# Optimization experiments

Measured on AMD Instinct MI355X. Metric: run time of the kernel, lower is better.

The kernel has to match this reference:

```python
import jax, jax.numpy as jnp
import numpy as np
from jax import lax

RADIUS = 8
EPS = 0.01


def box_filter(x, r):
    # Sum over a (2r+1)x(2r+1) window with zero ('same') padding — identical math
    # to depthwise conv2d with a ones kernel and padding=r.
    k = 2 * r + 1
    return lax.reduce_window(
        x, jnp.array(0, x.dtype), lax.add,
        window_dimensions=(1, 1, k, k),
        window_strides=(1, 1, 1, 1),
        padding=((0, 0), (0, 0), (r, r), (r, r)),
    )


def setup_inputs() -> dict:
    key = jax.random.key(0)
    k1, k2 = jax.random.split(key)
    shape = (16, 3, 512, 512)
    I = jax.random.uniform(k1, shape, dtype=jnp.float32)
    p = jax.random.uniform(k2, shape, dtype=jnp.float32)
    return {"I": I, "p": p}


def reference(I, p):
    r = RADIUS
    eps = EPS
    N = box_filter(jnp.ones_like(I), r)          # window pixel counts (handles borders)
    mean_I = box_filter(I, r) / N
    mean_p = box_filter(p, r) / N
    mean_Ip = box_filter(I * p, r) / N
    cov_Ip = mean_Ip - mean_I * mean_p
    mean_II = box_filter(I * I, r) / N
    var_I = mean_II - mean_I * mean_I
    a = cov_Ip / (var_I + eps)
    b = mean_p - a * mean_I
    mean_a = box_filter(a, r) / N
    mean_b = box_filter(b, r) / N
    q = mean_a * I + mean_b
    return q
```

## Files before the change

kernel.cpp:

```cpp
#include <hip/hip_runtime.h>


#define RAD  8
#define H    512
#define W    512
#define TILE 32
#define EPS  0.01f

__global__ __launch_bounds__(512, 4)
void guided_filter_kernel(const float* __restrict__ Ig,
                          const float* __restrict__ Pg,
                          float* __restrict__ out)
{
    __shared__ __align__(16) float4 F4[64 * 32];
    __shared__ __align__(16) float4 H4[64 * 48];

    float2* F2p = (float2*)F4;
    float2* AB  = (float2*)F4;
    float2* HAB = (float2*)F4 + 48 * 50;

    const int tid   = threadIdx.x;
    const int plane = blockIdx.z;
    const int x0 = blockIdx.x * TILE - 2 * RAD;
    const int y0 = blockIdx.y * TILE - 2 * RAD;
    const float* Ib = Ig + (size_t)plane * (H * W);
    const float* Pb = Pg + (size_t)plane * (H * W);
    float* Ob = out + (size_t)plane * (H * W);

    const bool interior = (x0 >= 0) && (y0 >= 0) && (x0 + 64 <= W) && (y0 + 64 <= H);
    if (interior) {
        #pragma unroll
        for (int it = 0; it < 2; ++it) {
            int idx = it * 512 + tid;
            int ry = idx >> 4, f4 = idx & 15;
            int rl = ry & 7, pf = ry & 1;
            const float* ip = Ib + (y0 + ry) * W + x0 + 4 * f4;
            const float* pp = Pb + (y0 + ry) * W + x0 + 4 * f4;
            float4 iv = *(const float4*)ip;
            float4 pv = *(const float4*)pp;
            float2 e0 = make_float2(iv.x, pv.x), e1 = make_float2(iv.y, pv.y);
            float2 e2 = make_float2(iv.z, pv.z), e3 = make_float2(iv.w, pv.w);
            float2 a0 = pf ? e1 : e0, a1 = pf ? e0 : e1;
            float2 b0 = pf ? e3 : e2, b1 = pf ? e2 : e3;
            float4* Fr = &F4[ry * 32];
            Fr[(2 * f4) ^ rl]     = make_float4(a0.x, a0.y, a1.x, a1.y);
            Fr[(2 * f4 + 1) ^ rl] = make_float4(b0.x, b0.y, b1.x, b1.y);
        }
    } else {
        #pragma unroll
        for (int it = 0; it < 2; ++it) {
            int idx = it * 512 + tid;
            int ry = idx >> 4, f4 = idx & 15;
            int rl = ry & 7, pf = ry & 1;
            int gy = y0 + ry;
            float2 el[4];
            #pragma unroll
            for (int k = 0; k < 4; ++k) {
                int gx = x0 + 4 * f4 + k;
                bool v = ((unsigned)gy < (unsigned)H) && ((unsigned)gx < (unsigned)W);
                el[k].x = v ? Ib[gy * W + gx] : 0.f;
                el[k].y = v ? Pb[gy * W + gx] : 0.f;
            }
            float2 a0 = pf ? el[1] : el[0], a1 = pf ? el[0] : el[1];
            float2 b0 = pf ? el[3] : el[2], b1 = pf ? el[2] : el[3];
            float4* Fr = &F4[ry * 32];
            Fr[(2 * f4) ^ rl]     = make_float4(a0.x, a0.y, a1.x, a1.y);
            Fr[(2 * f4 + 1) ^ rl] = make_float4(b0.x, b0.y, b1.x, b1.y);
        }
    }
    __syncthreads();

    {
        const int r  = tid >> 3, e = tid & 7;
        const int rl = r & 7, pf = r & 1;
        const int c0 = 6 * e;
        const float4* Fr = &F4[r * 32];
        const float2* Er = &F2p[r * 64];
        float4 S = make_float4(0.f, 0.f, 0.f, 0.f);
        const int g0 = 3 * e;
        #pragma unroll
        for (int m = 0; m < 8; ++m) {
            float4 g = Fr[(g0 + m) ^ rl];
            S.x += g.x + g.z;
            S.y += g.y + g.w;
            S.z += g.x * g.y + g.z * g.w;
            S.w += g.x * g.x + g.z * g.z;
        }
        {
            int c = c0 + 16;
            float2 v = Er[(((c >> 1) ^ rl) << 1) | pf];
            S.x += v.x; S.y += v.y; S.z += v.x * v.y; S.w += v.x * v.x;
        }
        #pragma unroll
        for (int k = 0; k < 6; ++k) {
            H4[r * 48 + ((c0 + k) ^ rl)] = S;
            if (k < 5) {
                int ca = c0 + k + 17, cs = c0 + k;
                float2 va = Er[(((ca >> 1) ^ rl) << 1) | ((ca & 1) ^ pf)];
                float2 vs = Er[(((cs >> 1) ^ rl) << 1) | ((cs & 1) ^ pf)];
                S.x += va.x - vs.x;
                S.y += va.y - vs.y;
                S.z += va.x * va.y - vs.x * vs.y;
                S.w += va.x * va.x - vs.x * vs.x;
            }
        }
    }
    __syncthreads();

    if (tid < 384) {
        const int col = tid % 48, chunk = tid / 48;
        const int cy0 = chunk * 6;
        float4 S = make_float4(0.f, 0.f, 0.f, 0.f);
        #pragma unroll
        for (int j = 0; j < 17; ++j) {
            int row = cy0 + j;
            float4 v = H4[row * 48 + (col ^ (row & 7))];
            S.x += v.x; S.y += v.y; S.z += v.z; S.w += v.w;
        }
        int gx = x0 + RAD + col;
        int nx = min(gx + RAD, W - 1) - max(gx - RAD, 0) + 1;
        #pragma unroll
        for (int k = 0; k < 6; ++k) {
            int cy = cy0 + k;
            int gy = y0 + RAD + cy;
            float a = 0.f, b = 0.f;
            if (((unsigned)gy < (unsigned)H) && ((unsigned)gx < (unsigned)W)) {
                int ny = min(gy + RAD, H - 1) - max(gy - RAD, 0) + 1;
                float invN = __builtin_amdgcn_rcpf((float)(nx * ny));
                float mI = S.x * invN, mp = S.y * invN;
                float cov = S.z * invN - mI * mp;
                float var = S.w * invN - mI * mI;
                a = cov * __builtin_amdgcn_rcpf(var + EPS);
                b = mp - a * mI;
            }
            AB[cy * 50 + col] = make_float2(a, b);
            if (k < 5) {
                int ra = cy + 17, rs = cy;
                float4 va = H4[ra * 48 + (col ^ (ra & 7))];
                float4 vs = H4[rs * 48 + (col ^ (rs & 7))];
                S.x += va.x - vs.x; S.y += va.y - vs.y;
                S.z += va.z - vs.z; S.w += va.w - vs.w;
            }
        }
    }
    __syncthreads();

    if (tid < 384) {
        const int r = tid % 48, e = tid / 48;
        const int c0 = 4 * e;
        const float2* row  = &AB[r * 50];
        const float4* rowg = (const float4*)row;
        float2 S = make_float2(0.f, 0.f);
        #pragma unroll
        for (int m = 0; m < 8; ++m) {
            float4 g = rowg[2 * e + m];
            S.x += g.x + g.z;
            S.y += g.y + g.w;
        }
        {
            float2 v = row[c0 + 16];
            S.x += v.x; S.y += v.y;
        }
        #pragma unroll
        for (int k = 0; k < 4; ++k) {
            HAB[r * 33 + c0 + k] = S;
            if (k < 3) {
                float2 va = row[c0 + k + 17];
                float2 vs = row[c0 + k];
                S.x += va.x - vs.x; S.y += va.y - vs.y;
            }
        }
    }
    __syncthreads();

    {
        const int col = tid & 31, chunk = tid >> 5;
        const int oy0 = chunk * 2;
        float2 S = make_float2(0.f, 0.f);
        #pragma unroll
        for (int j = 0; j < 17; ++j) {
            float2 v = HAB[(oy0 + j) * 33 + col];
            S.x += v.x; S.y += v.y;
        }
        int gx = x0 + 2 * RAD + col;
        int nx = min(gx + RAD, W - 1) - max(gx - RAD, 0) + 1;
        #pragma unroll
        for (int k = 0; k < 2; ++k) {
            int oy = oy0 + k;
            int gy = y0 + 2 * RAD + oy;
            int ny = min(gy + RAD, H - 1) - max(gy - RAD, 0) + 1;
            float invN = __builtin_amdgcn_rcpf((float)(nx * ny));
            float iv = Ib[gy * W + gx];
            Ob[gy * W + gx] = S.x * invN * iv + S.y * invN;
            if (k < 1) {
                float2 va = HAB[(oy + 17) * 33 + col];
                float2 vs = HAB[oy * 33 + col];
                S.x += va.x - vs.x; S.y += va.y - vs.y;
            }
        }
    }
}

extern "C" void kernel_launch(void* const* d_in, const int* in_sizes, int n_in,
                              void* d_out, int out_size, void* d_ws, size_t ws_size,
                              hipStream_t stream) {
    const float* I = (const float*)d_in[0];
    const float* P = (const float*)d_in[1];
    float* out = (float*)d_out;
    int planes = in_sizes[0] / (H * W);
    dim3 grid(W / TILE, H / TILE, planes);
    guided_filter_kernel<<<grid, dim3(512), 0, stream>>>(I, P, out);
}
```

Before: 247.8 us.

## Stream four vertical tiles per block with a rolling row-sum ring buffer

Each block now processes a column strip of four 32-row tiles. The horizontal row sums are kept in a 64-row ring buffer, so only 32 new raw rows are staged and row-summed per tile instead of recomputing the full 64-row halo. This cuts redundant vertical-halo loads and first-pass box-filter work. The cost is fewer blocks in the grid, which lowers parallelism, plus a serial chain of syncs inside each block.

```diff
diff --git a/kernel.cpp b/kernel.cpp
--- a/kernel.cpp
+++ b/kernel.cpp
@@ -5,6 +5,7 @@
 #define H    512
 #define W    512
 #define TILE 32
+#define KCH  4
 #define EPS  0.01f
 
 __global__ __launch_bounds__(512, 4)
@@ -22,158 +23,165 @@
     const int tid   = threadIdx.x;
     const int plane = blockIdx.z;
     const int x0 = blockIdx.x * TILE - 2 * RAD;
-    const int y0 = blockIdx.y * TILE - 2 * RAD;
+    const int Y0 = blockIdx.y * (TILE * KCH);
     const float* Ib = Ig + (size_t)plane * (H * W);
     const float* Pb = Pg + (size_t)plane * (H * W);
     float* Ob = out + (size_t)plane * (H * W);
 
-    const bool interior = (x0 >= 0) && (y0 >= 0) && (x0 + 64 <= W) && (y0 + 64 <= H);
-    if (interior) {
-        #pragma unroll
-        for (int it = 0; it < 2; ++it) {
-            int idx = it * 512 + tid;
-            int ry = idx >> 4, f4 = idx & 15;
-            int rl = ry & 7, pf = ry & 1;
-            const float* ip = Ib + (y0 + ry) * W + x0 + 4 * f4;
-            const float* pp = Pb + (y0 + ry) * W + x0 + 4 * f4;
-            float4 iv = *(const float4*)ip;
-            float4 pv = *(const float4*)pp;
-            float2 e0 = make_float2(iv.x, pv.x), e1 = make_float2(iv.y, pv.y);
-            float2 e2 = make_float2(iv.z, pv.z), e3 = make_float2(iv.w, pv.w);
-            float2 a0 = pf ? e1 : e0, a1 = pf ? e0 : e1;
-            float2 b0 = pf ? e3 : e2, b1 = pf ? e2 : e3;
-            float4* Fr = &F4[ry * 32];
-            Fr[(2 * f4) ^ rl]     = make_float4(a0.x, a0.y, a1.x, a1.y);
-            Fr[(2 * f4 + 1) ^ rl] = make_float4(b0.x, b0.y, b1.x, b1.y);
-        }
-    } else {
-        #pragma unroll
-        for (int it = 0; it < 2; ++it) {
-            int idx = it * 512 + tid;
-            int ry = idx >> 4, f4 = idx & 15;
-            int rl = ry & 7, pf = ry & 1;
-            int gy = y0 + ry;
-            float2 el[4];
+    auto stage_raw = [&](int ybase, int nrows) {
+        const int iters = (nrows * 16) >> 9;
+        const bool interior = (x0 >= 0) && (x0 + 64 <= W) &&
+                              (ybase >= 0) && (ybase + nrows <= H);
+        if (interior) {
+            for (int it = 0; it < iters; ++it) {
+                int idx = it * 512 + tid;
+                int ry = idx >> 4, f4 = idx & 15;
+                int rl = ry & 7, pf = ry & 1;
+                const float* ip = Ib + (ybase + ry) * W + x0 + 4 * f4;
+                const float* pp = Pb + (ybase + ry) * W + x0 + 4 * f4;
+                float4 iv = *(const float4*)ip;
+                float4 pv = *(const float4*)pp;
+                float2 e0 = make_float2(iv.x, pv.x), e1 = make_float2(iv.y, pv.y);
+                float2 e2 = make_float2(iv.z, pv.z), e3 = make_float2(iv.w, pv.w);
+                float2 a0 = pf ? e1 : e0, a1 = pf ? e0 : e1;
+                float2 b0 = pf ? e3 : e2, b1 = pf ? e2 : e3;
+                float4* Fr = &F4[ry * 32];
+                Fr[(2 * f4) ^ rl]     = make_float4(a0.x, a0.y, a1.x, a1.y);
+                Fr[(2 * f4 + 1) ^ rl] = make_float4(b0.x, b0.y, b1.x, b1.y);
+            }
+        } else {
+            for (int it = 0; it < iters; ++it) {
+                int idx = it * 512 + tid;
+                int ry = idx >> 4, f4 = idx & 15;
+                int rl = ry & 7, pf = ry & 1;
+                int gy = ybase + ry;
+                float2 el[4];
+                #pragma unroll
+                for (int k = 0; k < 4; ++k) {
+                    int gx = x0 + 4 * f4 + k;
+                    bool v = ((unsigned)gy < (unsigned)H) && ((unsigned)gx < (unsigned)W);
+                    el[k].x = v ? Ib[gy * W + gx] : 0.f;
+                    el[k].y = v ? Pb[gy * W + gx] : 0.f;
+                }
+                float2 a0 = pf ? el[1] : el[0], a1 = pf ? el[0] : el[1];
+                float2 b0 = pf ? el[3] : el[2], b1 = pf ? el[2] : el[3];
+                float4* Fr = &F4[ry * 32];
+                Fr[(2 * f4) ^ rl]     = make_float4(a0.x, a0.y, a1.x, a1.y);
+                Fr[(2 * f4 + 1) ^ rl] = make_float4(b0.x, b0.y, b1.x, b1.y);
+            }
+        }
+    };
+
+    auto s2_rows = [&](int tbase, bool full) {
+        if (full || tid < 256) {
+            const int r  = tid >> 3, e = tid & 7;
+            const int rl = r & 7, pf = r & 1;
+            const int c0 = 6 * e;
+            const float4* Fr = &F4[r * 32];
+            const float2* Er = (const float2*)Fr;
+            float4 S = make_float4(0.f, 0.f, 0.f, 0.f);
+            const int gb = 3 * e;
+            #pragma unroll
+            for (int m = 0; m < 8; ++m) {
+                float4 fr = Fr[(gb + m) ^ rl];
+                S.x += fr.x + fr.z;
+                S.y += fr.y + fr.w;
+                S.z += fr.x * fr.y + fr.z * fr.w;
+                S.w += fr.x * fr.x + fr.z * fr.z;
+            }
+            {
+                int c = c0 + 16;
+                float2 v = Er[(((c >> 1) ^ rl) << 1) | pf];
+                S.x += v.x; S.y += v.y; S.z += v.x * v.y; S.w += v.x * v.x;
+            }
+            const int slot = (tbase + r) & 63;
+            float4* Hrow = &H4[slot * 48];
+            #pragma unroll
+            for (int k = 0; k < 6; ++k) {
+                Hrow[(c0 + k) ^ rl] = S;
+                if (k < 5) {
+                    int ca = c0 + k + 17, cs = c0 + k;
+                    float2 va = Er[(((ca >> 1) ^ rl) << 1) | ((ca & 1) ^ pf)];
+                    float2 vs = Er[(((cs >> 1) ^ rl) << 1) | ((cs & 1) ^ pf)];
+                    S.x += va.x - vs.x;
+                    S.y += va.y - vs.y;
+                    S.z += va.x * va.y - vs.x * vs.y;
+                    S.w += va.x * va.x - vs.x * vs.x;
+                }
+            }
+        }
+    };
+
+    auto s3g = [&](int g) {
+        if (tid < 384) {
+            const int col = tid % 48, chunk = tid / 48;
+            const int cy0 = chunk * 6;
+            const int tb = 32 * g;
+            float4 S = make_float4(0.f, 0.f, 0.f, 0.f);
+            #pragma unroll
+            for (int j = 0; j < 17; ++j) {
+                int row = tb + cy0 + j;
+                float4 v = H4[(row & 63) * 48 + (col ^ (row & 7))];
+                S.x += v.x; S.y += v.y; S.z += v.z; S.w += v.w;
+            }
+            int gx = x0 + RAD + col;
+            int nx = min(gx + RAD, W - 1) - max(gx - RAD, 0) + 1;
+            #pragma unroll
+            for (int k = 0; k < 6; ++k) {
+                int cy = cy0 + k;
+                int gy = Y0 + 32 * g - RAD + cy;
+                float a = 0.f, b = 0.f;
+                if (((unsigned)gy < (unsigned)H) && ((unsigned)gx < (unsigned)W)) {
+                    int ny = min(gy + RAD, H - 1) - max(gy - RAD, 0) + 1;
+                    float invN = __builtin_amdgcn_rcpf((float)(nx * ny));
+                    float mI = S.x * invN, mp = S.y * invN;
+                    float cov = S.z * invN - mI * mp;
+                    float var = S.w * invN - mI * mI;
+                    a = cov * __builtin_amdgcn_rcpf(var + EPS);
+                    b = mp - a * mI;
+                }
+                AB[cy * 50 + col] = make_float2(a, b);
+                if (k < 5) {
+                    int ra = tb + cy + 17, rs = tb + cy;
+                    float4 va = H4[(ra & 63) * 48 + (col ^ (ra & 7))];
+                    float4 vs = H4[(rs & 63) * 48 + (col ^ (rs & 7))];
+                    S.x += va.x - vs.x; S.y += va.y - vs.y;
+                    S.z += va.z - vs.z; S.w += va.w - vs.w;
+                }
+            }
+        }
+    };
+
+    auto s4 = [&]() {
+        if (tid < 384) {
+            const int r = tid % 48, e = tid / 48;
+            const int c0 = 4 * e;
+            const float2* row  = &AB[r * 50];
+            const float4* rowg = (const float4*)row;
+            float2 S = make_float2(0.f, 0.f);
+            #pragma unroll
+            for (int m = 0; m < 8; ++m) {
+                float4 gq = rowg[2 * e + m];
+                S.x += gq.x + gq.z;
+                S.y += gq.y + gq.w;
+            }
+            {
+                float2 v = row[c0 + 16];
+                S.x += v.x; S.y += v.y;
+            }
             #pragma unroll
             for (int k = 0; k < 4; ++k) {
-                int gx = x0 + 4 * f4 + k;
-                bool v = ((unsigned)gy < (unsigned)H) && ((unsigned)gx < (unsigned)W);
-                el[k].x = v ? Ib[gy * W + gx] : 0.f;
-                el[k].y = v ? Pb[gy * W + gx] : 0.f;
-            }
-            float2 a0 = pf ? el[1] : el[0], a1 = pf ? el[0] : el[1];
-            float2 b0 = pf ? el[3] : el[2], b1 = pf ? el[2] : el[3];
-            float4* Fr = &F4[ry * 32];
-            Fr[(2 * f4) ^ rl]     = make_float4(a0.x, a0.y, a1.x, a1.y);
-            Fr[(2 * f4 + 1) ^ rl] = make_float4(b0.x, b0.y, b1.x, b1.y);
-        }
-    }
-    __syncthreads();
-
-    {
-        const int r  = tid >> 3, e = tid & 7;
-        const int rl = r & 7, pf = r & 1;
-        const int c0 = 6 * e;
-        const float4* Fr = &F4[r * 32];
-        const float2* Er = &F2p[r * 64];
-        float4 S = make_float4(0.f, 0.f, 0.f, 0.f);
-        const int g0 = 3 * e;
-        #pragma unroll
-        for (int m = 0; m < 8; ++m) {
-            float4 g = Fr[(g0 + m) ^ rl];
-            S.x += g.x + g.z;
-            S.y += g.y + g.w;
-            S.z += g.x * g.y + g.z * g.w;
-            S.w += g.x * g.x + g.z * g.z;
-        }
-        {
-            int c = c0 + 16;
-            float2 v = Er[(((c >> 1) ^ rl) << 1) | pf];
-            S.x += v.x; S.y += v.y; S.z += v.x * v.y; S.w += v.x * v.x;
-        }
-        #pragma unroll
-        for (int k = 0; k < 6; ++k) {
-            H4[r * 48 + ((c0 + k) ^ rl)] = S;
-            if (k < 5) {
-                int ca = c0 + k + 17, cs = c0 + k;
-                float2 va = Er[(((ca >> 1) ^ rl) << 1) | ((ca & 1) ^ pf)];
-                float2 vs = Er[(((cs >> 1) ^ rl) << 1) | ((cs & 1) ^ pf)];
-                S.x += va.x - vs.x;
-                S.y += va.y - vs.y;
-                S.z += va.x * va.y - vs.x * vs.y;
-                S.w += va.x * va.x - vs.x * vs.x;
-            }
-        }
-    }
-    __syncthreads();
-
-    if (tid < 384) {
-        const int col = tid % 48, chunk = tid / 48;
-        const int cy0 = chunk * 6;
-        float4 S = make_float4(0.f, 0.f, 0.f, 0.f);
-        #pragma unroll
-        for (int j = 0; j < 17; ++j) {
-            int row = cy0 + j;
-            float4 v = H4[row * 48 + (col ^ (row & 7))];
-            S.x += v.x; S.y += v.y; S.z += v.z; S.w += v.w;
-        }
-        int gx = x0 + RAD + col;
-        int nx = min(gx + RAD, W - 1) - max(gx - RAD, 0) + 1;
-        #pragma unroll
-        for (int k = 0; k < 6; ++k) {
-            int cy = cy0 + k;
-            int gy = y0 + RAD + cy;
-            float a = 0.f, b = 0.f;
-            if (((unsigned)gy < (unsigned)H) && ((unsigned)gx < (unsigned)W)) {
-                int ny = min(gy + RAD, H - 1) - max(gy - RAD, 0) + 1;
-                float invN = __builtin_amdgcn_rcpf((float)(nx * ny));
-                float mI = S.x * invN, mp = S.y * invN;
-                float cov = S.z * invN - mI * mp;
-                float var = S.w * invN - mI * mI;
-                a = cov * __builtin_amdgcn_rcpf(var + EPS);
-                b = mp - a * mI;
-            }
-            AB[cy * 50 + col] = make_float2(a, b);
-            if (k < 5) {
-                int ra = cy + 17, rs = cy;
-                float4 va = H4[ra * 48 + (col ^ (ra & 7))];
-                float4 vs = H4[rs * 48 + (col ^ (rs & 7))];
-                S.x += va.x - vs.x; S.y += va.y - vs.y;
-                S.z += va.z - vs.z; S.w += va.w - vs.w;
-            }
-        }
-    }
-    __syncthreads();
-
-    if (tid < 384) {
-        const int r = tid % 48, e = tid / 48;
-        const int c0 = 4 * e;
-        const float2* row  = &AB[r * 50];
-        const float4* rowg = (const float4*)row;
-        float2 S = make_float2(0.f, 0.f);
-        #pragma unroll
-        for (int m = 0; m < 8; ++m) {
-            float4 g = rowg[2 * e + m];
-            S.x += g.x + g.z;
-            S.y += g.y + g.w;
-        }
-        {
-            float2 v = row[c0 + 16];
-            S.x += v.x; S.y += v.y;
-        }
-        #pragma unroll
-        for (int k = 0; k < 4; ++k) {
-            HAB[r * 33 + c0 + k] = S;
-            if (k < 3) {
-                float2 va = row[c0 + k + 17];
-                float2 vs = row[c0 + k];
-                S.x += va.x - vs.x; S.y += va.y - vs.y;
-            }
-        }
-    }
-    __syncthreads();
-
-    {
+                HAB[r * 33 + c0 + k] = S;
+                if (k < 3) {
+                    float2 va = row[c0 + k + 17];
+                    float2 vs = row[c0 + k];
+                    S.x += va.x - vs.x; S.y += va.y - vs.y;
+                }
+            }
+        }
+    };
+
+    auto s5g = [&](int g) {
         const int col = tid & 31, chunk = tid >> 5;
         const int oy0 = chunk * 2;
         float2 S = make_float2(0.f, 0.f);
@@ -187,7 +195,7 @@
         #pragma unroll
         for (int k = 0; k < 2; ++k) {
             int oy = oy0 + k;
-            int gy = y0 + 2 * RAD + oy;
+            int gy = Y0 + 32 * g + oy;
             int ny = min(gy + RAD, H - 1) - max(gy - RAD, 0) + 1;
             float invN = __builtin_amdgcn_rcpf((float)(nx * ny));
             float iv = Ib[gy * W + gx];
@@ -198,6 +206,25 @@
                 S.x += va.x - vs.x; S.y += va.y - vs.y;
             }
         }
+    };
+
+    stage_raw(Y0 - 2 * RAD, 64);
+    __syncthreads();
+    s2_rows(0, true);
+    #pragma unroll 1
+    for (int g = 0; g < KCH; ++g) {
+        __syncthreads();
+        s3g(g);
+        __syncthreads();
+        s4();
+        __syncthreads();
+        if (g < KCH - 1)
+            stage_raw(Y0 + 32 * g + 48, 32);
+        s5g(g);
+        if (g < KCH - 1) {
+            __syncthreads();
+            s2_rows(32 * g + 64, false);
+        }
     }
 }
 
@@ -208,6 +235,6 @@
     const float* P = (const float*)d_in[1];
     float* out = (float*)d_out;
     int planes = in_sizes[0] / (H * W);
-    dim3 grid(W / TILE, H / TILE, planes);
+    dim3 grid(W / TILE, H / (TILE * KCH), planes);
     guided_filter_kernel<<<grid, dim3(512), 0, stream>>>(I, P, out);
 }
```

After: 242.4 us. 2.2% less time.

## Stream vertical tile chunks through a ring buffer with warp-specialized pipelined stages

Applied to the files above, without the earlier changes.

Each block now processes four vertically stacked 32-row tiles using a 48-row ring buffer of horizontal sums, so the vertical halo rows are shared instead of recomputed per tile. Thread groups are specialized so that the second box-filter stages of one chunk overlap with loading and first-stage sums of the next. The a/b intermediates are stored as half2 in shared memory to cut LDS footprint, which reduces the precision of the second filter pass. Block size and launch bounds change to 448 threads and 6 waves per EU, and the grid shrinks by the chunk factor.

```diff
diff --git a/kernel.cpp b/kernel.cpp
--- a/kernel.cpp
+++ b/kernel.cpp
@@ -1,203 +1,205 @@
 #include <hip/hip_runtime.h>
+#include <hip/hip_fp16.h>
 
 
 #define RAD  8
 #define H    512
 #define W    512
 #define TILE 32
+#define KCH  4
 #define EPS  0.01f
 
-__global__ __launch_bounds__(512, 4)
+__global__ __launch_bounds__(448, 6)
 void guided_filter_kernel(const float* __restrict__ Ig,
                           const float* __restrict__ Pg,
                           float* __restrict__ out)
 {
-    __shared__ __align__(16) float4 F4[64 * 32];
-    __shared__ __align__(16) float4 H4[64 * 48];
-
-    float2* F2p = (float2*)F4;
-    float2* AB  = (float2*)F4;
-    float2* HAB = (float2*)F4 + 48 * 50;
+    __shared__ __align__(16) float4  RING[48 * 48];
+    __shared__ __align__(8)  __half2 ABR[48 * 51];
+    __shared__ __align__(8)  __half2 HABR[48 * 33];
 
     const int tid   = threadIdx.x;
     const int plane = blockIdx.z;
     const int x0 = blockIdx.x * TILE - 2 * RAD;
-    const int y0 = blockIdx.y * TILE - 2 * RAD;
+    const int Y0 = blockIdx.y * (TILE * KCH);
     const float* Ib = Ig + (size_t)plane * (H * W);
     const float* Pb = Pg + (size_t)plane * (H * W);
     float* Ob = out + (size_t)plane * (H * W);
 
-    const bool interior = (x0 >= 0) && (y0 >= 0) && (x0 + 64 <= W) && (y0 + 64 <= H);
-    if (interior) {
-        #pragma unroll
-        for (int it = 0; it < 2; ++it) {
-            int idx = it * 512 + tid;
-            int ry = idx >> 4, f4 = idx & 15;
-            int rl = ry & 7, pf = ry & 1;
-            const float* ip = Ib + (y0 + ry) * W + x0 + 4 * f4;
-            const float* pp = Pb + (y0 + ry) * W + x0 + 4 * f4;
-            float4 iv = *(const float4*)ip;
-            float4 pv = *(const float4*)pp;
-            float2 e0 = make_float2(iv.x, pv.x), e1 = make_float2(iv.y, pv.y);
-            float2 e2 = make_float2(iv.z, pv.z), e3 = make_float2(iv.w, pv.w);
-            float2 a0 = pf ? e1 : e0, a1 = pf ? e0 : e1;
-            float2 b0 = pf ? e3 : e2, b1 = pf ? e2 : e3;
-            float4* Fr = &F4[ry * 32];
-            Fr[(2 * f4) ^ rl]     = make_float4(a0.x, a0.y, a1.x, a1.y);
-            Fr[(2 * f4 + 1) ^ rl] = make_float4(b0.x, b0.y, b1.x, b1.y);
-        }
-    } else {
-        #pragma unroll
-        for (int it = 0; it < 2; ++it) {
-            int idx = it * 512 + tid;
-            int ry = idx >> 4, f4 = idx & 15;
-            int rl = ry & 7, pf = ry & 1;
-            int gy = y0 + ry;
-            float2 el[4];
+    auto s2f = [&](int T0, int nrows, int tid2) {
+        if (tid2 < nrows * 8) {
+            const int r = tid2 >> 3, e = tid2 & 7;
+            int slot = (T0 % 48) + r; if (slot >= 48) slot -= 48;
+            const int rl = r & 7;
+            const int ty = Y0 + T0 - 16 + r;
+            const int cb = 6 * e;
+            float4 bI[6], bP[6];
+            const bool xint = (x0 >= 0) && (x0 + 64 <= W);
+            if (xint && ((unsigned)ty < (unsigned)H)) {
+                const float* pi = Ib + ty * W + x0 + cb;
+                const float* pp = Pb + ty * W + x0 + cb;
+                #pragma unroll
+                for (int k = 0; k < 6; ++k) {
+                    __builtin_memcpy(&bI[k], pi + 4 * k, 16);
+                    __builtin_memcpy(&bP[k], pp + 4 * k, 16);
+                }
+            } else {
+                const bool vy = (unsigned)ty < (unsigned)H;
+                float* fI = (float*)bI;
+                float* fP = (float*)bP;
+                #pragma unroll
+                for (int c = 0; c < 24; ++c) {
+                    int gx = x0 + cb + c;
+                    bool v = vy && ((unsigned)gx < (unsigned)W);
+                    fI[c] = v ? Ib[ty * W + gx] : 0.f;
+                    fP[c] = v ? Pb[ty * W + gx] : 0.f;
+                }
+            }
+            const float* fI = (const float*)bI;
+            const float* fP = (const float*)bP;
+            float4 S = make_float4(0.f, 0.f, 0.f, 0.f);
+            #pragma unroll
+            for (int c = 0; c <= 16; ++c) {
+                float iv = fI[c], pv = fP[c];
+                S.x += iv; S.y += pv; S.z += iv * pv; S.w += iv * iv;
+            }
+            float4* Hrow = &RING[slot * 48];
+            #pragma unroll
+            for (int k = 0; k < 6; ++k) {
+                Hrow[(cb + k) ^ rl] = S;
+                if (k < 5) {
+                    float ia = fI[17 + k], pa = fP[17 + k];
+                    float is = fI[k],      ps = fP[k];
+                    S.x += ia - is;
+                    S.y += pa - ps;
+                    S.z += ia * pa - is * ps;
+                    S.w += ia * ia - is * is;
+                }
+            }
+        }
+    };
+
+    auto s3 = [&](int AY, int nch) {
+        if (tid < 48 * nch) {
+            const int col = tid % 48;
+            const int ay0 = AY + 8 * (tid / 48);
+            const int base = ay0 % 48;
+            const int tW = 48 - base;
+            const char* Rb = (const char*)RING;
+            unsigned alo[8], ahi[8];
+            #pragma unroll
+            for (int k = 0; k < 8; ++k) {
+                alo[k] = (unsigned)(base * 768 + ((col ^ k) << 4));
+                ahi[k] = alo[k] - 36864u;
+            }
+            float4 S = make_float4(0.f, 0.f, 0.f, 0.f);
+            #pragma unroll
+            for (int j = 0; j < 17; ++j) {
+                unsigned off = (j >= tW ? ahi[j & 7] : alo[j & 7])
+                               + (unsigned)(j * 768);
+                float4 v = *(const float4*)(Rb + off);
+                S.x += v.x; S.y += v.y; S.z += v.z; S.w += v.w;
+            }
+            const int gx = x0 + RAD + col;
+            const int nx = min(gx + RAD, W - 1) - max(gx - RAD, 0) + 1;
+            #pragma unroll
+            for (int kk = 0; kk < 8; ++kk) {
+                int ya = Y0 + ay0 + kk - 8;
+                float a = 0.f, b = 0.f;
+                if (((unsigned)ya < (unsigned)H) && ((unsigned)gx < (unsigned)W)) {
+                    int ny = min(ya + RAD, H - 1) - max(ya - RAD, 0) + 1;
+                    float invN = __builtin_amdgcn_rcpf((float)(nx * ny));
+                    float mI = S.x * invN, mp = S.y * invN;
+                    float cov = S.z * invN - mI * mp;
+                    float var = S.w * invN - mI * mI;
+                    a = cov * __builtin_amdgcn_rcpf(var + EPS);
+                    b = mp - a * mI;
+                }
+                ABR[(base + kk) * 51 + col] = __floats2half2_rn(a, b);
+                if (kk < 7) {
+                    unsigned offs = (kk >= tW ? ahi[kk & 7] : alo[kk & 7])
+                                    + (unsigned)(kk * 768);
+                    int ja = kk + 17;
+                    unsigned offa = (ja >= tW ? ahi[ja & 7] : alo[ja & 7])
+                                    + (unsigned)(ja * 768);
+                    float4 va = *(const float4*)(Rb + offa);
+                    float4 vs = *(const float4*)(Rb + offs);
+                    S.x += va.x - vs.x; S.y += va.y - vs.y;
+                    S.z += va.z - vs.z; S.w += va.w - vs.w;
+                }
+            }
+        }
+    };
+
+    auto s4 = [&](int i) {
+        if (tid < 192) {
+            const int r = tid % 48, e = tid / 48;
+            const int c0 = 8 * e;
+            int slot = (32 * i) % 48 + r; if (slot >= 48) slot -= 48;
+            const __half2* Arow = &ABR[slot * 51];
+            float2 S = make_float2(0.f, 0.f);
+            #pragma unroll
+            for (int d = 0; d <= 16; ++d) {
+                float2 v = __half22float2(Arow[c0 + d]);
+                S.x += v.x; S.y += v.y;
+            }
+            #pragma unroll
+            for (int k = 0; k < 8; ++k) {
+                HABR[r * 33 + c0 + k] = __floats2half2_rn(S.x, S.y);
+                if (k < 7) {
+                    float2 va = __half22float2(Arow[c0 + k + 17]);
+                    float2 vs = __half22float2(Arow[c0 + k]);
+                    S.x += va.x - vs.x; S.y += va.y - vs.y;
+                }
+            }
+        }
+    };
+
+    auto s5 = [&](int i) {
+        if (tid >= 192) {
+            const int t2 = tid - 192;
+            const int qc = t2 & 31, oy0 = (t2 >> 5) * 4;
+            float2 S = make_float2(0.f, 0.f);
+            #pragma unroll
+            for (int j = 0; j < 17; ++j) {
+                float2 v = __half22float2(HABR[(oy0 + j) * 33 + qc]);
+                S.x += v.x; S.y += v.y;
+            }
+            const int gx = x0 + 2 * RAD + qc;
+            const int nx = min(gx + RAD, W - 1) - max(gx - RAD, 0) + 1;
             #pragma unroll
             for (int k = 0; k < 4; ++k) {
-                int gx = x0 + 4 * f4 + k;
-                bool v = ((unsigned)gy < (unsigned)H) && ((unsigned)gx < (unsigned)W);
-                el[k].x = v ? Ib[gy * W + gx] : 0.f;
-                el[k].y = v ? Pb[gy * W + gx] : 0.f;
-            }
-            float2 a0 = pf ? el[1] : el[0], a1 = pf ? el[0] : el[1];
-            float2 b0 = pf ? el[3] : el[2], b1 = pf ? el[2] : el[3];
-            float4* Fr = &F4[ry * 32];
-            Fr[(2 * f4) ^ rl]     = make_float4(a0.x, a0.y, a1.x, a1.y);
-            Fr[(2 * f4 + 1) ^ rl] = make_float4(b0.x, b0.y, b1.x, b1.y);
-        }
-    }
-    __syncthreads();
-
-    {
-        const int r  = tid >> 3, e = tid & 7;
-        const int rl = r & 7, pf = r & 1;
-        const int c0 = 6 * e;
-        const float4* Fr = &F4[r * 32];
-        const float2* Er = &F2p[r * 64];
-        float4 S = make_float4(0.f, 0.f, 0.f, 0.f);
-        const int g0 = 3 * e;
-        #pragma unroll
-        for (int m = 0; m < 8; ++m) {
-            float4 g = Fr[(g0 + m) ^ rl];
-            S.x += g.x + g.z;
-            S.y += g.y + g.w;
-            S.z += g.x * g.y + g.z * g.w;
-            S.w += g.x * g.x + g.z * g.z;
-        }
-        {
-            int c = c0 + 16;
-            float2 v = Er[(((c >> 1) ^ rl) << 1) | pf];
-            S.x += v.x; S.y += v.y; S.z += v.x * v.y; S.w += v.x * v.x;
-        }
-        #pragma unroll
-        for (int k = 0; k < 6; ++k) {
-            H4[r * 48 + ((c0 + k) ^ rl)] = S;
-            if (k < 5) {
-                int ca = c0 + k + 17, cs = c0 + k;
-                float2 va = Er[(((ca >> 1) ^ rl) << 1) | ((ca & 1) ^ pf)];
-                float2 vs = Er[(((cs >> 1) ^ rl) << 1) | ((cs & 1) ^ pf)];
-                S.x += va.x - vs.x;
-                S.y += va.y - vs.y;
-                S.z += va.x * va.y - vs.x * vs.y;
-                S.w += va.x * va.x - vs.x * vs.x;
-            }
-        }
-    }
-    __syncthreads();
-
-    if (tid < 384) {
-        const int col = tid % 48, chunk = tid / 48;
-        const int cy0 = chunk * 6;
-        float4 S = make_float4(0.f, 0.f, 0.f, 0.f);
-        #pragma unroll
-        for (int j = 0; j < 17; ++j) {
-            int row = cy0 + j;
-            float4 v = H4[row * 48 + (col ^ (row & 7))];
-            S.x += v.x; S.y += v.y; S.z += v.z; S.w += v.w;
-        }
-        int gx = x0 + RAD + col;
-        int nx = min(gx + RAD, W - 1) - max(gx - RAD, 0) + 1;
-        #pragma unroll
-        for (int k = 0; k < 6; ++k) {
-            int cy = cy0 + k;
-            int gy = y0 + RAD + cy;
-            float a = 0.f, b = 0.f;
-            if (((unsigned)gy < (unsigned)H) && ((unsigned)gx < (unsigned)W)) {
+                int gy = Y0 + 32 * i + oy0 + k;
                 int ny = min(gy + RAD, H - 1) - max(gy - RAD, 0) + 1;
                 float invN = __builtin_amdgcn_rcpf((float)(nx * ny));
-                float mI = S.x * invN, mp = S.y * invN;
-                float cov = S.z * invN - mI * mp;
-                float var = S.w * invN - mI * mI;
-                a = cov * __builtin_amdgcn_rcpf(var + EPS);
-                b = mp - a * mI;
-            }
-            AB[cy * 50 + col] = make_float2(a, b);
-            if (k < 5) {
-                int ra = cy + 17, rs = cy;
-                float4 va = H4[ra * 48 + (col ^ (ra & 7))];
-                float4 vs = H4[rs * 48 + (col ^ (rs & 7))];
-                S.x += va.x - vs.x; S.y += va.y - vs.y;
-                S.z += va.z - vs.z; S.w += va.w - vs.w;
-            }
-        }
-    }
-    __syncthreads();
-
-    if (tid < 384) {
-        const int r = tid % 48, e = tid / 48;
-        const int c0 = 4 * e;
-        const float2* row  = &AB[r * 50];
-        const float4* rowg = (const float4*)row;
-        float2 S = make_float2(0.f, 0.f);
-        #pragma unroll
-        for (int m = 0; m < 8; ++m) {
-            float4 g = rowg[2 * e + m];
-            S.x += g.x + g.z;
-            S.y += g.y + g.w;
-        }
-        {
-            float2 v = row[c0 + 16];
-            S.x += v.x; S.y += v.y;
-        }
-        #pragma unroll
-        for (int k = 0; k < 4; ++k) {
-            HAB[r * 33 + c0 + k] = S;
-            if (k < 3) {
-                float2 va = row[c0 + k + 17];
-                float2 vs = row[c0 + k];
-                S.x += va.x - vs.x; S.y += va.y - vs.y;
-            }
-        }
-    }
-    __syncthreads();
-
-    {
-        const int col = tid & 31, chunk = tid >> 5;
-        const int oy0 = chunk * 2;
-        float2 S = make_float2(0.f, 0.f);
-        #pragma unroll
-        for (int j = 0; j < 17; ++j) {
-            float2 v = HAB[(oy0 + j) * 33 + col];
-            S.x += v.x; S.y += v.y;
-        }
-        int gx = x0 + 2 * RAD + col;
-        int nx = min(gx + RAD, W - 1) - max(gx - RAD, 0) + 1;
-        #pragma unroll
-        for (int k = 0; k < 2; ++k) {
-            int oy = oy0 + k;
-            int gy = y0 + 2 * RAD + oy;
-            int ny = min(gy + RAD, H - 1) - max(gy - RAD, 0) + 1;
-            float invN = __builtin_amdgcn_rcpf((float)(nx * ny));
-            float iv = Ib[gy * W + gx];
-            Ob[gy * W + gx] = S.x * invN * iv + S.y * invN;
-            if (k < 1) {
-                float2 va = HAB[(oy + 17) * 33 + col];
-                float2 vs = HAB[oy * 33 + col];
-                S.x += va.x - vs.x; S.y += va.y - vs.y;
-            }
-        }
+                float iv = Ib[gy * W + gx];
+                Ob[gy * W + gx] = S.x * invN * iv + S.y * invN;
+                if (k < 3) {
+                    float2 va = __half22float2(HABR[(oy0 + k + 17) * 33 + qc]);
+                    float2 vs = __half22float2(HABR[(oy0 + k) * 33 + qc]);
+                    S.x += va.x - vs.x; S.y += va.y - vs.y;
+                }
+            }
+        }
+    };
+
+    s2f(0, 48, tid);
+    __syncthreads();
+    s3(0, 4);
+    __syncthreads();
+    s2f(48, 16, tid);
+    __syncthreads();
+    s3(32, 2);
+    __syncthreads();
+
+    #pragma unroll 1
+    for (int i = 0; i < KCH; ++i) {
+        if (tid < 192) s4(i);
+        else if (i < KCH - 1) s2f(32 * i + 64, 32, tid - 192);
+        __syncthreads();
+        if (tid < 192) { if (i < KCH - 1) s3(32 * i + 48, 4); }
+        else s5(i);
+        __syncthreads();
     }
 }
 
@@ -208,6 +210,6 @@
     const float* P = (const float*)d_in[1];
     float* out = (float*)d_out;
     int planes = in_sizes[0] / (H * W);
-    dim3 grid(W / TILE, H / TILE, planes);
-    guided_filter_kernel<<<grid, dim3(512), 0, stream>>>(I, P, out);
+    dim3 grid(W / TILE, H / (TILE * KCH), planes);
+    guided_filter_kernel<<<grid, dim3(448), 0, stream>>>(I, P, out);
 }
```

Measured after the change: 308.2 us. +24.4%, slower.
